# Kernel optimization log

Measured on AMD Instinct MI355X. Metric: run time of the kernel, lower is better.

## Reference

```python
import jax, jax.numpy as jnp
import numpy as np

N = 1024  # feature_size == hidden_size == n_nodes
K = 3     # diffusion hops
B = 2048  # batch


def setup_inputs() -> dict:
    key = jax.random.key(0)
    ks = jax.random.split(key, 32)

    # --- adjacency -> normalized K-hop filter list (constants in torch, requires_grad=False) ---
    A = jax.random.uniform(ks[0], (N, N), dtype=jnp.float32) + jnp.eye(N, dtype=jnp.float32)
    # D_inverse = diag(1/sum(A, 0)); norm_A = D_inverse @ A  -> row i scaled by 1/colsum[i]
    norm_A = A / jnp.sum(A, axis=0)[:, None]
    A_temp = jnp.eye(N, dtype=jnp.float32)
    hops = []
    for _ in range(K):
        A_temp = jnp.minimum(A_temp @ norm_A, 1.0)  # Clamp_A: clamp(max=1.0)
        hops.append(A_temp)
    A_list = jnp.stack(hops)  # [K, N, N]

    stdv = 1.0 / np.sqrt(N)
    gin = K * N + 2 * N  # gc_input_size + hidden*2
    rin = N + 2 * N      # input_size + hidden*2

    def U(k, shape, fan_in):
        s = 1.0 / np.sqrt(fan_in)
        return jax.random.uniform(k, shape, jnp.float32, -s, s)

    inp = {
        "input": jax.random.normal(ks[1], (B, N), jnp.float32),
        "input_t": jax.random.normal(ks[2], (B, N), jnp.float32),
        "Hidden_State": jax.random.normal(ks[3], (B, N), jnp.float32),
        "Cell_State": jax.random.normal(ks[4], (B, N), jnp.float32),
        "rHidden_State": jax.random.normal(ks[5], (B, N), jnp.float32),
        "rCell_State": jax.random.normal(ks[6], (B, N), jnp.float32),
        "pred": jax.random.normal(ks[7], (B, N), jnp.float32),
        "A_list": A_list,
        "gc_W": U(ks[8], (K, N, N), N),  # FilterLinear weights (masked by A_list)
        "fl_W": U(ks[9], (N, gin), gin), "fl_b": U(ks[10], (N,), gin),
        "il_W": U(ks[11], (N, gin), gin), "il_b": U(ks[12], (N,), gin),
        "ol_W": U(ks[13], (N, gin), gin), "ol_b": U(ks[14], (N,), gin),
        "Cl_W": U(ks[15], (N, gin), gin), "Cl_b": U(ks[16], (N,), gin),
        "Neighbor_weight": jax.random.uniform(ks[17], (N,), jnp.float32, -stdv, stdv),
        "rfl_W": U(ks[18], (N, rin), rin), "rfl_b": U(ks[19], (N,), rin),
        "ril_W": U(ks[20], (N, rin), rin), "ril_b": U(ks[21], (N,), rin),
        "rol_W": U(ks[22], (N, rin), rin), "rol_b": U(ks[23], (N,), rin),
        "rCl_W": U(ks[24], (N, rin), rin), "rCl_b": U(ks[25], (N,), rin),
        "c": jnp.ones((1,), jnp.float32),
    }
    return inp


def reference(input, input_t, Hidden_State, Cell_State, rHidden_State, rCell_State, pred,
              A_list, gc_W, fl_W, fl_b, il_W, il_b, ol_W, ol_b, Cl_W, Cl_b,
              Neighbor_weight, rfl_W, rfl_b, ril_W, ril_b, rol_W, rol_b, rCl_W, rCl_b, c):
    # K-hop masked graph convolutions: gc_k = x @ (A_k * W_k)^T, concatenated -> [B, K*N]
    gc = jnp.einsum('bn,kmn->bkm', input, A_list * gc_W).reshape(B, K * N)

    combined = jnp.concatenate([gc, Hidden_State, pred], axis=1)  # [B, K*N + 2N]
    f = jax.nn.sigmoid(combined @ fl_W.T + fl_b)
    i = jax.nn.sigmoid(combined @ il_W.T + il_b)
    o = jax.nn.sigmoid(combined @ ol_W.T + ol_b)
    C = jnp.tanh(combined @ Cl_W.T + Cl_b)

    # NC = Cell_State * (A_list[-1] @ Neighbor_weight), broadcast over batch
    NC = Cell_State * (A_list[-1] @ Neighbor_weight)
    Cell = f * NC + i * C
    Hidden = o * jnp.tanh(Cell)

    rcombined = jnp.concatenate([input_t, rHidden_State, pred], axis=1)  # [B, 3N]
    rf = jax.nn.sigmoid(rcombined @ rfl_W.T + rfl_b)
    ri = jax.nn.sigmoid(rcombined @ ril_W.T + ril_b)
    ro = jax.nn.sigmoid(rcombined @ rol_W.T + rol_b)
    rC = jnp.tanh(rcombined @ rCl_W.T + rCl_b)
    rCell = rf * rCell_State + ri * rC
    rHidden = ro * jnp.tanh(rCell)

    # torch.var is unbiased (ddof=1)
    var1 = jnp.var(input_t[:, :N], ddof=1)
    var2 = jnp.var(gc, ddof=1)
    pred_new = (Hidden * var1 * c + rHidden[:, :N] * var2) / (var1 + var2 * c)

    Hidden_out = Hidden - pred_new
    # rHidden has exactly N columns, so rHidden[:, N:] is empty -> just subtract
    rHidden_out = rHidden - pred_new
    return (Hidden_out, Cell, gc, rHidden_out, rCell, pred_new)
```

## Files before the change

kernel.cpp:

```cpp
#include <hip/hip_runtime.h>
#include <cstdint>
#include <cstddef>

typedef unsigned short u16;
typedef __attribute__((ext_vector_type(8))) __bf16 bf16x8;
typedef __attribute__((ext_vector_type(4))) float f32x4;

#define DEV __device__ __forceinline__

DEV u16 f2bf(float f) {
  unsigned u = __float_as_uint(f);
  return (u16)((u + 0x7FFFu + ((u >> 16) & 1u)) >> 16);
}
DEV float bf2f(u16 b) { return __uint_as_float((unsigned)b << 16); }

DEV void glds16(const void* g, void* l) {
  __builtin_amdgcn_global_load_lds((const __attribute__((address_space(1))) void*)g,
                                   (__attribute__((address_space(3))) void*)l,
                                   16, 0, 0);
}

#define BAR() __builtin_amdgcn_s_barrier()
#define SB() __builtin_amdgcn_sched_barrier(0)
#define LGK0() asm volatile("s_waitcnt lgkmcnt(0)" ::: "memory")
#define VM(n) asm volatile("s_waitcnt vmcnt(" #n ")" ::: "memory")

#define PREP_GRID 13088

__global__ void prep_all(
    const float* __restrict__ input, const float* __restrict__ input_t,
    const float* __restrict__ HS, const float* __restrict__ rHS,
    const float* __restrict__ pred, const float* __restrict__ A_list,
    const float* __restrict__ gc_W,
    const float* __restrict__ fl_W, const float* __restrict__ il_W,
    const float* __restrict__ ol_W, const float* __restrict__ Cl_W,
    const float* __restrict__ rfl_W, const float* __restrict__ ril_W,
    const float* __restrict__ rol_W, const float* __restrict__ rCl_W,
    const float* __restrict__ fl_b, const float* __restrict__ il_b,
    const float* __restrict__ ol_b, const float* __restrict__ Cl_b,
    const float* __restrict__ rfl_b, const float* __restrict__ ril_b,
    const float* __restrict__ rol_b, const float* __restrict__ rCl_b,
    const float* __restrict__ Nw,
    u16* __restrict__ bA, u16* __restrict__ comb, u16* __restrict__ rcomb,
    u16* __restrict__ AW, u16* __restrict__ gW, u16* __restrict__ rW,
    float* __restrict__ bias_g, float* __restrict__ bias_r,
    float* __restrict__ nvec, float* __restrict__ part1) {
  __shared__ float red[16];
  const int bid = blockIdx.x, tid = threadIdx.x;

  if (bid < 512) {
    for (int i = bid * 256 + tid; i < 524288; i += 131072) {
      float4 v = *(const float4*)(input + (size_t)i * 4);
      *(ushort4*)(bA + (size_t)i * 4) =
          make_ushort4(f2bf(v.x), f2bf(v.y), f2bf(v.z), f2bf(v.w));
    }
  } else if (bid < 2560) {
    int b = bid - 512;
    int j = tid << 2;
    float4 v = *(const float4*)(input_t + (size_t)b * 1024 + j);
    *(ushort4*)(rcomb + (size_t)b * 3072 + j) =
        make_ushort4(f2bf(v.x), f2bf(v.y), f2bf(v.z), f2bf(v.w));
    float ls = v.x + v.y + v.z + v.w;
    float lq = v.x * v.x + v.y * v.y + v.z * v.z + v.w * v.w;
#pragma unroll
    for (int off = 32; off; off >>= 1) { ls += __shfl_down(ls, off); lq += __shfl_down(lq, off); }
    if ((tid & 63) == 0) { int w = tid >> 6; red[w] = ls; red[8 + w] = lq; }
    __syncthreads();
    if (tid == 0) {
      part1[(size_t)b * 2]     = red[0] + red[1] + red[2] + red[3];
      part1[(size_t)b * 2 + 1] = red[8] + red[9] + red[10] + red[11];
    }
  } else if (bid < 3072) {
    for (int i = (bid - 2560) * 256 + tid; i < 524288; i += 131072) {
      int b = i >> 8, j = (i & 255) << 2;
      float4 v = *(const float4*)(HS + (size_t)b * 1024 + j);
      *(ushort4*)(comb + (size_t)b * 5120 + 3072 + j) =
          make_ushort4(f2bf(v.x), f2bf(v.y), f2bf(v.z), f2bf(v.w));
    }
  } else if (bid < 3584) {
    for (int i = (bid - 3072) * 256 + tid; i < 524288; i += 131072) {
      int b = i >> 8, j = (i & 255) << 2;
      float4 v = *(const float4*)(rHS + (size_t)b * 1024 + j);
      *(ushort4*)(rcomb + (size_t)b * 3072 + 1024 + j) =
          make_ushort4(f2bf(v.x), f2bf(v.y), f2bf(v.z), f2bf(v.w));
    }
  } else if (bid < 4096) {
    for (int i = (bid - 3584) * 256 + tid; i < 524288; i += 131072) {
      int b = i >> 8, j = (i & 255) << 2;
      float4 v = *(const float4*)(pred + (size_t)b * 1024 + j);
      ushort4 u = make_ushort4(f2bf(v.x), f2bf(v.y), f2bf(v.z), f2bf(v.w));
      *(ushort4*)(comb + (size_t)b * 5120 + 4096 + j) = u;
      *(ushort4*)(rcomb + (size_t)b * 3072 + 2048 + j) = u;
    }
  } else if (bid < 4864) {
    for (long i = (long)(bid - 4096) * 256 + tid; i < 786432; i += 768L * 256) {
      float4 va = *(const float4*)(A_list + i * 4);
      float4 vw = *(const float4*)(gc_W + i * 4);
      *(ushort4*)(AW + i * 4) = make_ushort4(f2bf(va.x * vw.x), f2bf(va.y * vw.y),
                                             f2bf(va.z * vw.z), f2bf(va.w * vw.w));
    }
  } else if (bid < 8960) {
    int q = bid - 4864;
    int seg = q >> 10, tb = q & 1023;
    const float* s = (seg == 0) ? fl_W : (seg == 1) ? il_W : (seg == 2) ? ol_W : Cl_W;
    u16* dd = gW + (size_t)seg * 5242880;
    for (long i = (long)tb * 256 + tid; i < 1310720; i += 1024L * 256) {
      float4 v = *(const float4*)(s + i * 4);
      *(ushort4*)(dd + i * 4) = make_ushort4(f2bf(v.x), f2bf(v.y), f2bf(v.z), f2bf(v.w));
    }
  } else if (bid < 12032) {
    int q = bid - 8960;
    int seg = q / 768, tb = q - seg * 768;
    const float* s = (seg == 0) ? rfl_W : (seg == 1) ? ril_W : (seg == 2) ? rol_W : rCl_W;
    u16* dd = rW + (size_t)seg * 3145728;
    for (long i = (long)tb * 256 + tid; i < 786432; i += 768L * 256) {
      float4 v = *(const float4*)(s + i * 4);
      *(ushort4*)(dd + i * 4) = make_ushort4(f2bf(v.x), f2bf(v.y), f2bf(v.z), f2bf(v.w));
    }
  } else if (bid < 12064) {
    int i = (bid - 12032) * 256 + tid;
    int seg = i >> 10;
    const float* s = (seg == 0) ? fl_b : (seg == 1) ? il_b : (seg == 2) ? ol_b : (seg == 3) ? Cl_b
                   : (seg == 4) ? rfl_b : (seg == 5) ? ril_b : (seg == 6) ? rol_b : rCl_b;
    float v = s[i & 1023];
    if (i < 4096) bias_g[i] = v; else bias_r[i - 4096] = v;
  } else {
    int m = bid - 12064;
    const float* A3 = A_list + 2L * 1024 * 1024;
    float s = 0.f;
    for (int c = tid; c < 1024; c += 256) s += A3[(size_t)m * 1024 + c] * Nw[c];
#pragma unroll
    for (int off = 32; off; off >>= 1) s += __shfl_down(s, off);
    if ((tid & 63) == 0) red[tid >> 6] = s;
    __syncthreads();
    if (tid == 0) nvec[m] = red[0] + red[1] + red[2] + red[3];
  }
}

__global__ void reduce_sums(const float* __restrict__ p1, int n1,
                            const float* __restrict__ p2, int n2,
                            float* __restrict__ sums) {
  float a = 0.f, b = 0.f, c = 0.f, d = 0.f;
  for (int i = threadIdx.x; i < n1; i += 256) { a += p1[2 * i]; b += p1[2 * i + 1]; }
  for (int i = threadIdx.x; i < n2; i += 256) { c += p2[2 * i]; d += p2[2 * i + 1]; }
#pragma unroll
  for (int off = 32; off; off >>= 1) {
    a += __shfl_down(a, off); b += __shfl_down(b, off);
    c += __shfl_down(c, off); d += __shfl_down(d, off);
  }
  __shared__ float red[16];
  if ((threadIdx.x & 63) == 0) {
    int w = threadIdx.x >> 6;
    red[w] = a; red[4 + w] = b; red[8 + w] = c; red[12 + w] = d;
  }
  __syncthreads();
  if (threadIdx.x == 0) {
    sums[0] = red[0] + red[1] + red[2] + red[3];
    sums[1] = red[4] + red[5] + red[6] + red[7];
    sums[2] = red[8] + red[9] + red[10] + red[11];
    sums[3] = red[12] + red[13] + red[14] + red[15];
  }
}

__launch_bounds__(256)
__global__ void gemm_bt(const u16* __restrict__ A, int lda,
                        const u16* __restrict__ W, int ldw, int K,
                        float* __restrict__ out0, int ld0,
                        u16* __restrict__ outb, int ldb,
                        float* __restrict__ partials) {
  __shared__ u16 lA[128 * 64];
  __shared__ u16 lB[128 * 64];
  const int tid = threadIdx.x;
  const int w = tid >> 6, l = tid & 63;
  const int bm = blockIdx.y << 7, bn = blockIdx.x << 7;
  const int waveM = ((w >> 1) & 1) << 6, waveN = (w & 1) << 6;
  const int quad = l >> 4, r16 = l & 15;

  const int srow = l >> 3;
  const int schunk = (l & 7) ^ srow;
  const u16* gA = A + (size_t)(bm + w * 32 + srow) * lda + schunk * 8;
  const u16* gB = W + (size_t)(bn + w * 32 + srow) * ldw + schunk * 8;
  u16* sA = lA + (w * 32) * 64;
  u16* sB = lB + (w * 32) * 64;

  f32x4 acc[4][4] = {};

  for (int k0 = 0; k0 < K; k0 += 64) {
#pragma unroll
    for (int i = 0; i < 4; i++) {
      glds16(gA + (size_t)(i * 8) * lda + k0, sA + i * 8 * 64);
      glds16(gB + (size_t)(i * 8) * ldw + k0, sB + i * 8 * 64);
    }
    __syncthreads();
#pragma unroll
    for (int ks = 0; ks < 2; ks++) {
      bf16x8 av[4], bv[4];
#pragma unroll
      for (int mi = 0; mi < 4; mi++) {
        int row = waveM + mi * 16 + r16;
        int ch = (ks * 4 + quad) ^ (r16 & 7);
        av[mi] = *(const bf16x8*)(lA + row * 64 + ch * 8);
      }
#pragma unroll
      for (int ni = 0; ni < 4; ni++) {
        int row = waveN + ni * 16 + r16;
        int ch = (ks * 4 + quad) ^ (r16 & 7);
        bv[ni] = *(const bf16x8*)(lB + row * 64 + ch * 8);
      }
#pragma unroll
      for (int mi = 0; mi < 4; mi++)
#pragma unroll
        for (int ni = 0; ni < 4; ni++)
          acc[mi][ni] = __builtin_amdgcn_mfma_f32_16x16x32_bf16(av[mi], bv[ni], acc[mi][ni], 0, 0, 0);
    }
    __syncthreads();
  }

  float ls = 0.f, lq = 0.f;
#pragma unroll
  for (int mi = 0; mi < 4; mi++)
#pragma unroll
    for (int ni = 0; ni < 4; ni++) {
      int col = bn + waveN + ni * 16 + r16;
#pragma unroll
      for (int e = 0; e < 4; e++) {
        int row = bm + waveM + mi * 16 + quad * 4 + e;
        float v = acc[mi][ni][e];
        out0[(size_t)row * ld0 + col] = v;
        outb[(size_t)row * ldb + col] = f2bf(v);
        ls += v;
        lq += v * v;
      }
    }
#pragma unroll
  for (int off = 32; off; off >>= 1) { ls += __shfl_down(ls, off); lq += __shfl_down(lq, off); }
  __shared__ float red[8];
  if (l == 0) { red[w] = ls; red[4 + w] = lq; }
  __syncthreads();
  if (tid == 0) {
    int bidx = blockIdx.y * gridDim.x + blockIdx.x;
    partials[(size_t)bidx * 2]     = red[0] + red[1] + red[2] + red[3];
    partials[(size_t)bidx * 2 + 1] = red[4] + red[5] + red[6] + red[7];
  }
}

__launch_bounds__(512, 2)
__global__ void gemm_fused(const u16* __restrict__ comb, const u16* __restrict__ gW,
                           const u16* __restrict__ rcomb, const u16* __restrict__ rW,
                           u16* __restrict__ gp2a, u16* __restrict__ gp2b,
                           u16* __restrict__ gp3) {
  __shared__ __attribute__((aligned(16))) u16 sm[2 * 32768];
  const int tid = threadIdx.x;
  const int w = tid >> 6, l = tid & 63;
  const int quad = l >> 4, r16 = l & 15;
  const int sr = w >> 1, sc = w & 1;
  const int b = blockIdx.x;
  const int h = b & 1, t = b >> 1;
  const int ty = t & 7, tx = t >> 3;
  const int bm = ty << 8, bn = tx << 8;
  const int srow = tid >> 3;
  const int schunk = (tid & 7) ^ (srow & 7);

  auto run = [&](const u16* Abase, int lda, const u16* Wbase, int ldw,
                 int kBegin, int NT, u16* outp) {
    const u16* gA = Abase + (size_t)(bm + srow) * lda + schunk * 8 + kBegin;
    const u16* gB = Wbase + (size_t)(bn + srow) * ldw + schunk * 8 + kBegin;

    f32x4 acc[2][2][2][4];
#pragma unroll
    for (int a = 0; a < 2; a++)
#pragma unroll
      for (int c = 0; c < 2; c++)
#pragma unroll
        for (int mi = 0; mi < 2; mi++)
#pragma unroll
          for (int ni = 0; ni < 4; ni++) acc[a][c][mi][ni] = f32x4{0.f, 0.f, 0.f, 0.f};

    bf16x8 av0[2][2], av1[2][2], bv[4][2];

    auto stageA = [&](int buf, int hA, int T) {
      const u16* g = gA + (size_t)(hA * 128) * lda + (size_t)T * 64;
      u16* d = sm + buf * 32768 + hA * 8192 + tid * 8;
      glds16(g, d);
      glds16(g + (size_t)64 * lda, d + 4096);
    };
    auto stageB = [&](int buf, int hB, int T) {
      const u16* g = gB + (size_t)(hB * 128) * ldw + (size_t)T * 64;
      u16* d = sm + buf * 32768 + 16384 + hB * 8192 + tid * 8;
      glds16(g, d);
      glds16(g + (size_t)64 * ldw, d + 4096);
    };
    auto rdA = [&](int buf, int qr) {
      const u16* base = sm + buf * 32768;
#pragma unroll
      for (int mi = 0; mi < 2; mi++)
#pragma unroll
        for (int ks = 0; ks < 2; ks++) {
          int row = qr * 128 + sr * 32 + mi * 16 + r16;
          int ch = (ks * 4 + quad) ^ (r16 & 7);
          bf16x8 v = *(const bf16x8*)(base + row * 64 + ch * 8);
          if (qr) av1[mi][ks] = v; else av0[mi][ks] = v;
        }
    };
    auto rdB = [&](int buf, int qc) {
      const u16* base = sm + buf * 32768 + 16384;
#pragma unroll
      for (int ni = 0; ni < 4; ni++)
#pragma unroll
        for (int ks = 0; ks < 2; ks++) {
          int row = qc * 128 + sc * 64 + ni * 16 + r16;
          int ch = (ks * 4 + quad) ^ (r16 & 7);
          bv[ni][ks] = *(const bf16x8*)(base + row * 64 + ch * 8);
        }
    };
    auto mf = [&](int qr, int qc) {
      __builtin_amdgcn_s_setprio(1);
#pragma unroll
      for (int ks = 0; ks < 2; ks++)
#pragma unroll
        for (int mi = 0; mi < 2; mi++)
#pragma unroll
          for (int ni = 0; ni < 4; ni++)
            acc[qr][qc][mi][ni] = __builtin_amdgcn_mfma_f32_16x16x32_bf16(
                qr ? av1[mi][ks] : av0[mi][ks], bv[ni][ks], acc[qr][qc][mi][ni], 0, 0, 0);
      __builtin_amdgcn_s_setprio(0);
    };

    stageB(0, 0, 0); stageA(0, 0, 0); stageA(0, 1, 0); stageB(0, 1, 0);
    stageB(1, 0, 1); stageA(1, 0, 1);
    SB(); VM(8); BAR(); SB();

#pragma unroll 1
    for (int T = 0; T < NT - 2; T++) {
      const int cur = T & 1, nxt = cur ^ 1;
      rdA(cur, 0); rdB(cur, 0);
      stageA(nxt, 1, T + 1);
      SB(); VM(8); BAR(); SB();
      LGK0(); SB();
      mf(0, 0);
      BAR(); SB();
      rdA(cur, 1);
      stageB(nxt, 1, T + 1);
      SB(); VM(8); BAR(); SB();
      LGK0(); SB();
      mf(1, 0);
      BAR(); SB();
      rdB(cur, 1);
      stageB(cur, 0, T + 2);
      SB(); BAR(); SB();
      LGK0(); SB();
      mf(0, 1);
      BAR(); SB();
      stageA(cur, 0, T + 2);
      SB(); VM(8); BAR(); SB();
      mf(1, 1);
      BAR(); SB();
    }
    {
      const int cur = (NT - 2) & 1, nxt = cur ^ 1;
      rdA(cur, 0); rdB(cur, 0);
      stageA(nxt, 1, NT - 1);
      SB(); VM(8); BAR(); SB(); LGK0(); SB(); mf(0, 0); BAR(); SB();
      rdA(cur, 1);
      stageB(nxt, 1, NT - 1);
      SB(); VM(8); BAR(); SB(); LGK0(); SB(); mf(1, 0); BAR(); SB();
      rdB(cur, 1);
      SB(); BAR(); SB(); LGK0(); SB(); mf(0, 1); BAR(); SB();
      SB(); VM(4); BAR(); SB(); mf(1, 1); BAR(); SB();
    }
    {
      const int cur = (NT - 1) & 1;
      rdA(cur, 0); rdB(cur, 0);
      SB(); VM(2); BAR(); SB(); LGK0(); SB(); mf(0, 0); BAR(); SB();
      rdA(cur, 1);
      SB(); VM(0); BAR(); SB(); LGK0(); SB(); mf(1, 0); BAR(); SB();
      rdB(cur, 1);
      SB(); BAR(); SB(); LGK0(); SB(); mf(0, 1); BAR(); SB();
      mf(1, 1);
      BAR(); SB();
    }

#pragma unroll
    for (int qr = 0; qr < 2; qr++)
#pragma unroll
      for (int qc = 0; qc < 2; qc++)
#pragma unroll
        for (int mi = 0; mi < 2; mi++)
#pragma unroll
          for (int ni = 0; ni < 4; ni++) {
            int col = bn + qc * 128 + sc * 64 + ni * 16 + r16;
#pragma unroll
            for (int e = 0; e < 4; e++) {
              int row = bm + qr * 128 + sr * 32 + mi * 16 + quad * 4 + e;
              outp[(size_t)row * 4096 + col] = f2bf(acc[qr][qc][mi][ni][e]);
            }
          }
    SB(); VM(0); SB();
  };

  if (h == 0) {
    run(comb, 5120, gW, 5120, 0, 16, gp2a);
    run(rcomb, 3072, rW, 3072, 0, 48, gp3);
  } else {
    run(comb, 5120, gW, 5120, 1024, 64, gp2b);
  }
}


DEV float4 gate2(const u16* __restrict__ p0, const u16* __restrict__ p1,
                 const float* __restrict__ bias, size_t base, int boff) {
  ushort4 a = *(const ushort4*)(p0 + base);
  ushort4 b = *(const ushort4*)(p1 + base);
  float4 bb = *(const float4*)(bias + boff);
  return make_float4(bf2f(a.x) + bf2f(b.x) + bb.x, bf2f(a.y) + bf2f(b.y) + bb.y,
                     bf2f(a.z) + bf2f(b.z) + bb.z, bf2f(a.w) + bf2f(b.w) + bb.w);
}
DEV float4 gate1(const u16* __restrict__ p0, const float* __restrict__ bias,
                 size_t base, int boff) {
  ushort4 a = *(const ushort4*)(p0 + base);
  float4 bb = *(const float4*)(bias + boff);
  return make_float4(bf2f(a.x) + bb.x, bf2f(a.y) + bb.y, bf2f(a.z) + bb.z, bf2f(a.w) + bb.w);
}
DEV float4 sig4(float4 v) {
  return make_float4(1.f / (1.f + __expf(-v.x)), 1.f / (1.f + __expf(-v.y)),
                     1.f / (1.f + __expf(-v.z)), 1.f / (1.f + __expf(-v.w)));
}
DEV float4 tanh4(float4 v) {
  return make_float4(tanhf(v.x), tanhf(v.y), tanhf(v.z), tanhf(v.w));
}

__global__ void epilogue(const u16* __restrict__ gp2a, const u16* __restrict__ gp2b,
                         const u16* __restrict__ gp3,
                         const float* __restrict__ bias_g, const float* __restrict__ bias_r,
                         const float* __restrict__ CS, const float* __restrict__ rCS,
                         const float* __restrict__ nvec,
                         const float* __restrict__ sums, const float* __restrict__ cp,
                         float* __restrict__ Hout, float* __restrict__ CellOut,
                         float* __restrict__ rHout, float* __restrict__ rCellOut,
                         float* __restrict__ predOut) {
  const float n1 = 2097152.f, n2 = 6291456.f;
  float var1 = (sums[1] - sums[0] * sums[0] / n1) / (n1 - 1.f);
  float var2 = (sums[3] - sums[2] * sums[2] / n2) / (n2 - 1.f);
  float c = cp[0];
  float inv = 1.f / (var1 + var2 * c);
  float s1 = var1 * c, s2 = var2;

  int t = blockIdx.x * blockDim.x + threadIdx.x;
  int b = t >> 8, j = (t & 255) << 2;
  size_t rb = (size_t)b * 4096 + j;

  float4 f = sig4(gate2(gp2a, gp2b, bias_g, rb, j));
  float4 ii = sig4(gate2(gp2a, gp2b, bias_g, rb + 1024, 1024 + j));
  float4 o = sig4(gate2(gp2a, gp2b, bias_g, rb + 2048, 2048 + j));
  float4 C = tanh4(gate2(gp2a, gp2b, bias_g, rb + 3072, 3072 + j));
  float4 rf = sig4(gate1(gp3, bias_r, rb, j));
  float4 ri = sig4(gate1(gp3, bias_r, rb + 1024, 1024 + j));
  float4 ro = sig4(gate1(gp3, bias_r, rb + 2048, 2048 + j));
  float4 rC = tanh4(gate1(gp3, bias_r, rb + 3072, 3072 + j));

  float4 cs = *(const float4*)(CS + (size_t)b * 1024 + j);
  float4 rcs = *(const float4*)(rCS + (size_t)b * 1024 + j);
  float4 nv = *(const float4*)(nvec + j);

  float4 cell, hid, rcell, rhid, p, ho, rho;
  cell.x = f.x * (cs.x * nv.x) + ii.x * C.x; hid.x = o.x * tanhf(cell.x);
  cell.y = f.y * (cs.y * nv.y) + ii.y * C.y; hid.y = o.y * tanhf(cell.y);
  cell.z = f.z * (cs.z * nv.z) + ii.z * C.z; hid.z = o.z * tanhf(cell.z);
  cell.w = f.w * (cs.w * nv.w) + ii.w * C.w; hid.w = o.w * tanhf(cell.w);
  rcell.x = rf.x * rcs.x + ri.x * rC.x; rhid.x = ro.x * tanhf(rcell.x);
  rcell.y = rf.y * rcs.y + ri.y * rC.y; rhid.y = ro.y * tanhf(rcell.y);
  rcell.z = rf.z * rcs.z + ri.z * rC.z; rhid.z = ro.z * tanhf(rcell.z);
  rcell.w = rf.w * rcs.w + ri.w * rC.w; rhid.w = ro.w * tanhf(rcell.w);
  p.x = (hid.x * s1 + rhid.x * s2) * inv; ho.x = hid.x - p.x; rho.x = rhid.x - p.x;
  p.y = (hid.y * s1 + rhid.y * s2) * inv; ho.y = hid.y - p.y; rho.y = rhid.y - p.y;
  p.z = (hid.z * s1 + rhid.z * s2) * inv; ho.z = hid.z - p.z; rho.z = rhid.z - p.z;
  p.w = (hid.w * s1 + rhid.w * s2) * inv; ho.w = hid.w - p.w; rho.w = rhid.w - p.w;

  size_t i = (size_t)b * 1024 + j;
  *(float4*)(CellOut + i) = cell;
  *(float4*)(rCellOut + i) = rcell;
  *(float4*)(Hout + i) = ho;
  *(float4*)(rHout + i) = rho;
  *(float4*)(predOut + i) = p;
}


extern "C" void kernel_launch(void* const* d_in, const int* in_sizes, int n_in,
                              void* d_out, int out_size, void* d_ws, size_t ws_size,
                              hipStream_t stream) {
  const float* input   = (const float*)d_in[0];
  const float* input_t = (const float*)d_in[1];
  const float* HS      = (const float*)d_in[2];
  const float* CS      = (const float*)d_in[3];
  const float* rHS     = (const float*)d_in[4];
  const float* rCS     = (const float*)d_in[5];
  const float* pred    = (const float*)d_in[6];
  const float* A_list  = (const float*)d_in[7];
  const float* gc_W    = (const float*)d_in[8];
  const float* fl_W  = (const float*)d_in[9];  const float* fl_b  = (const float*)d_in[10];
  const float* il_W  = (const float*)d_in[11]; const float* il_b  = (const float*)d_in[12];
  const float* ol_W  = (const float*)d_in[13]; const float* ol_b  = (const float*)d_in[14];
  const float* Cl_W  = (const float*)d_in[15]; const float* Cl_b  = (const float*)d_in[16];
  const float* Nw    = (const float*)d_in[17];
  const float* rfl_W = (const float*)d_in[18]; const float* rfl_b = (const float*)d_in[19];
  const float* ril_W = (const float*)d_in[20]; const float* ril_b = (const float*)d_in[21];
  const float* rol_W = (const float*)d_in[22]; const float* rol_b = (const float*)d_in[23];
  const float* rCl_W = (const float*)d_in[24]; const float* rCl_b = (const float*)d_in[25];
  const float* cp    = (const float*)d_in[26];

  float* out      = (float*)d_out;
  float* Hout     = out;
  float* CellOut  = out + 2097152;
  float* gcOut    = out + 4194304;
  float* rHout    = out + 10485760;
  float* rCellOut = out + 12582912;
  float* predOut  = out + 14680064;

  char* ws = (char*)d_ws;
  size_t off = 0;
  auto alloc = [&](size_t bytes) -> void* {
    void* p = ws + off;
    off = (off + bytes + 255) & ~(size_t)255;
    return p;
  };
  float* sums   = (float*)alloc(16);
  float* part1  = (float*)alloc(2048 * 2 * 4);
  float* part2  = (float*)alloc(384 * 2 * 4);
  float* nvec   = (float*)alloc(1024 * 4);
  float* bias_g = (float*)alloc(4096 * 4);
  float* bias_r = (float*)alloc(4096 * 4);
  u16* comb  = (u16*)alloc((size_t)2048 * 5120 * 2);
  u16* rcomb = (u16*)alloc((size_t)2048 * 3072 * 2);
  u16* AW    = (u16*)alloc((size_t)3 * 1024 * 1024 * 2);
  u16* gW    = (u16*)alloc((size_t)4096 * 5120 * 2);
  u16* rW    = (u16*)alloc((size_t)4096 * 3072 * 2);
  u16* gp2a  = (u16*)alloc((size_t)2048 * 4096 * 2);
  u16* gp2b  = (u16*)alloc((size_t)2048 * 4096 * 2);
  u16* gp3   = (u16*)alloc((size_t)2048 * 4096 * 2);
  u16* bA = (u16*)gp2a;

  prep_all<<<PREP_GRID, 256, 0, stream>>>(
      input, input_t, HS, rHS, pred, A_list, gc_W,
      fl_W, il_W, ol_W, Cl_W, rfl_W, ril_W, rol_W, rCl_W,
      fl_b, il_b, ol_b, Cl_b, rfl_b, ril_b, rol_b, rCl_b, Nw,
      bA, comb, rcomb, AW, gW, rW, bias_g, bias_r, nvec, part1);

  gemm_bt<<<dim3(24, 16), 256, 0, stream>>>(bA, 1024, AW, 1024, 1024,
                                            gcOut, 3072, comb, 5120, part2);
  reduce_sums<<<1, 256, 0, stream>>>(part1, 2048, part2, 384, sums);
  gemm_fused<<<256, 512, 0, stream>>>(comb, gW, rcomb, rW, gp2a, gp2b, gp3);
  epilogue<<<2048, 256, 0, stream>>>(gp2a, gp2b, gp3, bias_g, bias_r, CS, rCS, nvec,
                                     sums, cp, Hout, CellOut, rHout, rCellOut, predOut);

  (void)in_sizes; (void)n_in; (void)out_size; (void)ws_size;
}
```

Measured before the change: 444.1 us.

## Restructure GEMM main loop to stage full tile ahead and batch LDS reads

Replaces the fine-grained half-tile staging schedule with a simpler double-buffered scheme: each tile issues all eight global-to-LDS loads for the next K tile up front, reads all A and B fragments from LDS at once into separate register sets, and uses partial lgkmcnt waits to overlap the LDS reads with MFMA work. The aim is fewer vmcnt waits and barriers per tile and better overlap of LDS reads with matrix ops. In exchange it uses more fragment registers and waits for all of the next tile's global loads at the end of each tile, which may expose global latency the previous interleaved schedule had hidden.

```diff
diff --git a/kernel.cpp b/kernel.cpp
--- a/kernel.cpp
+++ b/kernel.cpp
@@ -22,8 +22,8 @@
 
 #define BAR() __builtin_amdgcn_s_barrier()
 #define SB() __builtin_amdgcn_sched_barrier(0)
-#define LGK0() asm volatile("s_waitcnt lgkmcnt(0)" ::: "memory")
-#define VM(n) asm volatile("s_waitcnt vmcnt(" #n ")" ::: "memory")
+#define LGKN(n) asm volatile("s_waitcnt lgkmcnt(" #n ")" ::: "memory")
+#define VM0() asm volatile("s_waitcnt vmcnt(0)" ::: "memory")
 
 #define PREP_GRID 13088
 
@@ -276,44 +276,38 @@
 #pragma unroll
           for (int ni = 0; ni < 4; ni++) acc[a][c][mi][ni] = f32x4{0.f, 0.f, 0.f, 0.f};
 
-    bf16x8 av0[2][2], av1[2][2], bv[4][2];
-
-    auto stageA = [&](int buf, int hA, int T) {
-      const u16* g = gA + (size_t)(hA * 128) * lda + (size_t)T * 64;
-      u16* d = sm + buf * 32768 + hA * 8192 + tid * 8;
-      glds16(g, d);
-      glds16(g + (size_t)64 * lda, d + 4096);
+    bf16x8 a0[2][2], a1[2][2], b0[4][2], b1[4][2];
+
+    auto stageAll = [&](int buf, int T) {
+      const size_t k0 = (size_t)T * 64;
+      u16* dA = sm + buf * 32768 + tid * 8;
+      u16* dB = sm + buf * 32768 + 16384 + tid * 8;
+      glds16(gA + k0, dA);
+      glds16(gA + (size_t)64 * lda + k0, dA + 4096);
+      glds16(gA + (size_t)128 * lda + k0, dA + 8192);
+      glds16(gA + (size_t)192 * lda + k0, dA + 12288);
+      glds16(gB + k0, dB);
+      glds16(gB + (size_t)64 * ldw + k0, dB + 4096);
+      glds16(gB + (size_t)128 * ldw + k0, dB + 8192);
+      glds16(gB + (size_t)192 * ldw + k0, dB + 12288);
     };
-    auto stageB = [&](int buf, int hB, int T) {
-      const u16* g = gB + (size_t)(hB * 128) * ldw + (size_t)T * 64;
-      u16* d = sm + buf * 32768 + 16384 + hB * 8192 + tid * 8;
-      glds16(g, d);
-      glds16(g + (size_t)64 * ldw, d + 4096);
+    auto rdA = [&](int buf, int qr, bf16x8 (&dst)[2][2]) {
+      const u16* base = sm + buf * 32768 + (qr * 128 + sr * 32 + r16) * 64;
+#pragma unroll
+      for (int mi = 0; mi < 2; mi++)
+#pragma unroll
+        for (int ks = 0; ks < 2; ks++)
+          dst[mi][ks] = *(const bf16x8*)(base + mi * 16 * 64 + (((ks * 4 + quad) ^ (r16 & 7))) * 8);
     };
-    auto rdA = [&](int buf, int qr) {
-      const u16* base = sm + buf * 32768;
-#pragma unroll
-      for (int mi = 0; mi < 2; mi++)
-#pragma unroll
-        for (int ks = 0; ks < 2; ks++) {
-          int row = qr * 128 + sr * 32 + mi * 16 + r16;
-          int ch = (ks * 4 + quad) ^ (r16 & 7);
-          bf16x8 v = *(const bf16x8*)(base + row * 64 + ch * 8);
-          if (qr) av1[mi][ks] = v; else av0[mi][ks] = v;
-        }
+    auto rdB = [&](int buf, int qc, bf16x8 (&dst)[4][2]) {
+      const u16* base = sm + buf * 32768 + 16384 + (qc * 128 + sc * 64 + r16) * 64;
+#pragma unroll
+      for (int ni = 0; ni < 4; ni++)
+#pragma unroll
+        for (int ks = 0; ks < 2; ks++)
+          dst[ni][ks] = *(const bf16x8*)(base + ni * 16 * 64 + (((ks * 4 + quad) ^ (r16 & 7))) * 8);
     };
-    auto rdB = [&](int buf, int qc) {
-      const u16* base = sm + buf * 32768 + 16384;
-#pragma unroll
-      for (int ni = 0; ni < 4; ni++)
-#pragma unroll
-        for (int ks = 0; ks < 2; ks++) {
-          int row = qc * 128 + sc * 64 + ni * 16 + r16;
-          int ch = (ks * 4 + quad) ^ (r16 & 7);
-          bv[ni][ks] = *(const bf16x8*)(base + row * 64 + ch * 8);
-        }
-    };
-    auto mf = [&](int qr, int qc) {
+    auto mf = [&](int qr, int qc, bf16x8 (&A)[2][2], bf16x8 (&B)[4][2]) {
       __builtin_amdgcn_s_setprio(1);
 #pragma unroll
       for (int ks = 0; ks < 2; ks++)
@@ -322,63 +316,37 @@
 #pragma unroll
           for (int ni = 0; ni < 4; ni++)
             acc[qr][qc][mi][ni] = __builtin_amdgcn_mfma_f32_16x16x32_bf16(
-                qr ? av1[mi][ks] : av0[mi][ks], bv[ni][ks], acc[qr][qc][mi][ni], 0, 0, 0);
+                A[mi][ks], B[ni][ks], acc[qr][qc][mi][ni], 0, 0, 0);
       __builtin_amdgcn_s_setprio(0);
     };
 
-    stageB(0, 0, 0); stageA(0, 0, 0); stageA(0, 1, 0); stageB(0, 1, 0);
-    stageB(1, 0, 1); stageA(1, 0, 1);
-    SB(); VM(8); BAR(); SB();
-
+    auto tile = [&](int buf, int T, bool doStage) {
+      if (doStage) stageAll(buf ^ 1, T + 1);
+      rdA(buf, 0, a0); rdB(buf, 0, b0); rdA(buf, 1, a1); rdB(buf, 1, b1);
+      SB(); LGKN(12); SB();
+      mf(0, 0, a0, b0);
+      BAR(); SB();
+      LGKN(8); SB();
+      mf(1, 0, a1, b0);
+      BAR(); SB();
+      LGKN(0); SB();
+      mf(0, 1, a0, b1);
+      BAR(); SB();
+      mf(1, 1, a1, b1);
+      SB(); VM0(); BAR(); SB();
+    };
+
+    stageAll(0, 0);
+    SB(); VM0(); BAR(); SB();
+
+    int T = 0;
 #pragma unroll 1
-    for (int T = 0; T < NT - 2; T++) {
-      const int cur = T & 1, nxt = cur ^ 1;
-      rdA(cur, 0); rdB(cur, 0);
-      stageA(nxt, 1, T + 1);
-      SB(); VM(8); BAR(); SB();
-      LGK0(); SB();
-      mf(0, 0);
-      BAR(); SB();
-      rdA(cur, 1);
-      stageB(nxt, 1, T + 1);
-      SB(); VM(8); BAR(); SB();
-      LGK0(); SB();
-      mf(1, 0);
-      BAR(); SB();
-      rdB(cur, 1);
-      stageB(cur, 0, T + 2);
-      SB(); BAR(); SB();
-      LGK0(); SB();
-      mf(0, 1);
-      BAR(); SB();
-      stageA(cur, 0, T + 2);
-      SB(); VM(8); BAR(); SB();
-      mf(1, 1);
-      BAR(); SB();
-    }
-    {
-      const int cur = (NT - 2) & 1, nxt = cur ^ 1;
-      rdA(cur, 0); rdB(cur, 0);
-      stageA(nxt, 1, NT - 1);
-      SB(); VM(8); BAR(); SB(); LGK0(); SB(); mf(0, 0); BAR(); SB();
-      rdA(cur, 1);
-      stageB(nxt, 1, NT - 1);
-      SB(); VM(8); BAR(); SB(); LGK0(); SB(); mf(1, 0); BAR(); SB();
-      rdB(cur, 1);
-      SB(); BAR(); SB(); LGK0(); SB(); mf(0, 1); BAR(); SB();
-      SB(); VM(4); BAR(); SB(); mf(1, 1); BAR(); SB();
-    }
-    {
-      const int cur = (NT - 1) & 1;
-      rdA(cur, 0); rdB(cur, 0);
-      SB(); VM(2); BAR(); SB(); LGK0(); SB(); mf(0, 0); BAR(); SB();
-      rdA(cur, 1);
-      SB(); VM(0); BAR(); SB(); LGK0(); SB(); mf(1, 0); BAR(); SB();
-      rdB(cur, 1);
-      SB(); BAR(); SB(); LGK0(); SB(); mf(0, 1); BAR(); SB();
-      mf(1, 1);
-      BAR(); SB();
-    }
+    for (; T + 2 < NT; T += 2) {
+      tile(0, T, true);
+      tile(1, T + 1, true);
+    }
+    tile(0, NT - 2, true);
+    tile(1, NT - 1, false);
 
 #pragma unroll
     for (int qr = 0; qr < 2; qr++)
@@ -395,7 +363,6 @@
               outp[(size_t)row * 4096 + col] = f2bf(acc[qr][qc][mi][ni][e]);
             }
           }
-    SB(); VM(0); SB();
   };
 
   if (h == 0) {
```

New measurement: 459.6 us. +3.5%, slower.
